# Performance work log

Measured on AMD Instinct MI355X. Metric: run time of the kernel, lower is better.

Reference implementation:

```python
import jax, jax.numpy as jnp
import numpy as np

H = 8          # num_heads
EPS = 1e-5     # nn.LayerNorm default eps


def _attn(x, kv, wq, bq, wk, bk, wv, bv, wo, bo):
    # x: [B, Nq, D] queries; kv: [B, Nk, D] keys/values. softmax over keys (dim=-1).
    B, Nq, D = x.shape
    Nk = kv.shape[1]
    d = D // H
    q = (x @ wq + bq).reshape(B, Nq, H, d).transpose(0, 2, 1, 3)   # [B,h,Nq,d]
    k = (kv @ wk + bk).reshape(B, Nk, H, d).transpose(0, 2, 1, 3)  # [B,h,Nk,d]
    v = (kv @ wv + bv).reshape(B, Nk, H, d).transpose(0, 2, 1, 3)  # [B,h,Nk,d]
    scores = jnp.einsum('bhqd,bhkd->bhqk', q, k) * (d ** -0.5)
    a = jax.nn.softmax(scores, axis=-1)                            # softmax_dim='keys'
    ctx = jnp.einsum('bhqk,bhkd->bhqd', a, v)
    ctx = ctx.transpose(0, 2, 1, 3).reshape(B, Nq, D)
    return ctx @ wo + bo


def _ln(x, g, b):
    mu = jnp.mean(x, axis=-1, keepdims=True)
    var = jnp.var(x, axis=-1, keepdims=True)  # biased, matches torch LayerNorm
    return (x - mu) * jax.lax.rsqrt(var + EPS) * g + b


def setup_inputs() -> dict:
    key = jax.random.key(0)
    B, Nq, Nk, D = 2, 2048, 4096, 512
    Hid = 4 * D
    ks = jax.random.split(key, 32)
    s = 0.02
    r = lambda i, shp: jax.random.normal(ks[i], shp, dtype=jnp.float32) * s
    inp = {
        'x': jax.random.normal(ks[0], (B, Nq, D), dtype=jnp.float32),
        'cross': jax.random.normal(ks[1], (B, Nk, D), dtype=jnp.float32),
        # cross-attention projections (stored as [in, out])
        'ca_wq': r(2, (D, D)), 'ca_bq': jnp.zeros((D,), jnp.float32),
        'ca_wk': r(3, (D, D)), 'ca_bk': jnp.zeros((D,), jnp.float32),
        'ca_wv': r(4, (D, D)), 'ca_bv': jnp.zeros((D,), jnp.float32),
        'ca_wo': r(5, (D, D)), 'ca_bo': jnp.zeros((D,), jnp.float32),
        # self-attention projections
        'sa_wq': r(6, (D, D)), 'sa_bq': jnp.zeros((D,), jnp.float32),
        'sa_wk': r(7, (D, D)), 'sa_bk': jnp.zeros((D,), jnp.float32),
        'sa_wv': r(8, (D, D)), 'sa_bv': jnp.zeros((D,), jnp.float32),
        'sa_wo': r(9, (D, D)), 'sa_bo': jnp.zeros((D,), jnp.float32),
        # layer norms
        'ln1_g': jnp.ones((D,), jnp.float32), 'ln1_b': jnp.zeros((D,), jnp.float32),
        'ln2_g': jnp.ones((D,), jnp.float32), 'ln2_b': jnp.zeros((D,), jnp.float32),
        # MLP
        'mlp_w1': r(10, (D, Hid)), 'mlp_b1': jnp.zeros((Hid,), jnp.float32),
        'mlp_w2': r(11, (Hid, D)), 'mlp_b2': jnp.zeros((D,), jnp.float32),
    }
    return inp


def reference(x, cross,
              ca_wq, ca_bq, ca_wk, ca_bk, ca_wv, ca_bv, ca_wo, ca_bo,
              sa_wq, sa_bq, sa_wk, sa_bk, sa_wv, sa_bv, sa_wo, sa_bo,
              ln1_g, ln1_b, ln2_g, ln2_b,
              mlp_w1, mlp_b1, mlp_w2, mlp_b2):
    # a) cross-attention
    xc = _attn(x, cross, ca_wq, ca_bq, ca_wk, ca_bk, ca_wv, ca_bv, ca_wo, ca_bo)
    # b,c) LN then self-attention (Q=K=V=ln1(xc))
    xn = _ln(xc, ln1_g, ln1_b)
    xs = _attn(xn, xn, sa_wq, sa_bq, sa_wk, sa_bk, sa_wv, sa_bv, sa_wo, sa_bo)
    # d) residual
    y = xc + xs
    # e,f) LN + GELU MLP (torch GELU default = exact erf)
    h1 = jax.nn.gelu(_ln(y, ln2_g, ln2_b) @ mlp_w1 + mlp_b1, approximate=False)
    z = h1 @ mlp_w2 + mlp_b2
    # g) residual
    return y + z
```

## Files before the change

### kernel.cpp

```cpp
#include <hip/hip_runtime.h>
#include <math.h>

typedef _Float16 f16;
typedef __attribute__((ext_vector_type(8))) _Float16 f16x8;
typedef __attribute__((ext_vector_type(4))) _Float16 f16x4;
typedef __attribute__((ext_vector_type(4))) float f32x4;

#define QSCALE 0.1803368801111204f

__device__ __forceinline__ void gl_lds16(const f16* g, f16* l) {
    __builtin_amdgcn_global_load_lds((const __attribute__((address_space(1))) void*)g,
                                     (__attribute__((address_space(3))) void*)l, 16, 0, 0);
}

__global__ __launch_bounds__(256)
void cvt_f16_kernel(const float* __restrict__ X, f16* __restrict__ Y) {
    size_t i = ((size_t)blockIdx.x * 256 + threadIdx.x) * 4;
    f32x4 v = *(const f32x4*)(X + i);
    f16x4 o;
    o[0] = (f16)v[0]; o[1] = (f16)v[1]; o[2] = (f16)v[2]; o[3] = (f16)v[3];
    *(f16x4*)(Y + i) = o;
}

__global__ __launch_bounds__(256)
void transpose_cvt(const float* __restrict__ W, f16* __restrict__ Wt, int K, int N) {
    __shared__ float t[32][33];
    int tx = threadIdx.x, ty = threadIdx.y;
    int n0 = blockIdx.x * 32, k0 = blockIdx.y * 32;
#pragma unroll
    for (int i = 0; i < 4; i++)
        t[ty + i * 8][tx] = W[(size_t)(k0 + ty + i * 8) * N + n0 + tx];
    __syncthreads();
#pragma unroll
    for (int i = 0; i < 4; i++)
        Wt[(size_t)(n0 + ty + i * 8) * K + k0 + tx] = (f16)t[tx][ty + i * 8];
}

struct P8 { const float* s[8]; f16* d[8]; };
__global__ __launch_bounds__(256)
void transpose_cvt8(P8 p) {
    __shared__ float t[32][33];
    const float* W = p.s[blockIdx.z];
    f16* Wt = p.d[blockIdx.z];
    int tx = threadIdx.x, ty = threadIdx.y;
    int n0 = blockIdx.x * 32, k0 = blockIdx.y * 32;
#pragma unroll
    for (int i = 0; i < 4; i++)
        t[ty + i * 8][tx] = W[(size_t)(k0 + ty + i * 8) * 512 + n0 + tx];
    __syncthreads();
#pragma unroll
    for (int i = 0; i < 4; i++)
        Wt[(size_t)(n0 + ty + i * 8) * 512 + k0 + tx] = (f16)t[tx][ty + i * 8];
}

__global__ __launch_bounds__(256)
void transpose_v(const f16* __restrict__ Vh, f16* __restrict__ Vt, int Nk) {
    __shared__ f16 t[64][72];
    int bh = blockIdx.y, k0 = blockIdx.x * 64;
    int tid = threadIdx.x;
    int kr = tid >> 2, dc = (tid & 3) * 16;
    const f16* src = Vh + ((size_t)bh * Nk + k0 + kr) * 64 + dc;
    f16x8 a = *(const f16x8*)src;
    f16x8 b = *(const f16x8*)(src + 8);
    *(f16x8*)&t[kr][dc] = a;
    *(f16x8*)&t[kr][dc + 8] = b;
    __syncthreads();
    int dr = tid >> 2, kc = (tid & 3) * 16;
    f16x8 o0, o1;
#pragma unroll
    for (int j = 0; j < 8; j++) { o0[j] = t[kc + j][dr]; o1[j] = t[kc + 8 + j][dr]; }
    f16* dst = Vt + ((size_t)bh * 64 + dr) * Nk + k0 + kc;
    *(f16x8*)dst = o0;
    *(f16x8*)(dst + 8) = o1;
}

__global__ __launch_bounds__(128)
void layernorm_f16(const float* __restrict__ X, const float* __restrict__ g,
                   const float* __restrict__ bta, f16* __restrict__ Y)
{
    __shared__ float red[4];
    int row = blockIdx.x;
    int tid = threadIdx.x;
    const float* x = X + (size_t)row * 512;
    f32x4 v = *(const f32x4*)(x + tid * 4);
    float s  = v[0] + v[1] + v[2] + v[3];
    float ss = v[0] * v[0] + v[1] * v[1] + v[2] * v[2] + v[3] * v[3];
#pragma unroll
    for (int m = 1; m < 64; m <<= 1) {
        s  += __shfl_xor(s, m, 64);
        ss += __shfl_xor(ss, m, 64);
    }
    int wave = tid >> 6, lane = tid & 63;
    if (lane == 0) { red[wave * 2] = s; red[wave * 2 + 1] = ss; }
    __syncthreads();
    s = red[0] + red[2]; ss = red[1] + red[3];
    float mu  = s * (1.0f / 512);
    float var = ss * (1.0f / 512) - mu * mu;
    float inv = rsqrtf(var + 1e-5f);
    f32x4 gv = *(const f32x4*)(g + tid * 4);
    f32x4 bv = *(const f32x4*)(bta + tid * 4);
    f16x4 o;
#pragma unroll
    for (int i = 0; i < 4; i++) o[i] = (f16)((v[i] - mu) * inv * gv[i] + bv[i]);
    *(f16x4*)(Y + (size_t)row * 512 + tid * 4) = o;
}

__global__ __launch_bounds__(256)
void gemm_f16(const f16* __restrict__ A, const f16* __restrict__ Wt,
              const float* __restrict__ b0, const float* __restrict__ b1,
              const float* __restrict__ b2, const float* __restrict__ res,
              float* __restrict__ Cf32, f16* __restrict__ C16,
              f16* __restrict__ hm0, f16* __restrict__ hm1, f16* __restrict__ hm2,
              int N, int K, int NBshift, int fused, int act, float s0)
{
    __shared__ __align__(16) f16 As[128 * 64];
    __shared__ __align__(16) f16 Bs[128 * 64];
    int tid = threadIdx.x, lane = tid & 63, wave = tid >> 6;
    int quad = lane >> 4, ln16 = lane & 15;
    int wm = wave >> 1, wn = wave & 1;
    int bm0 = blockIdx.y * 128, bn0 = blockIdx.x * 128;

    f32x4 acc[4][4];
#pragma unroll
    for (int i = 0; i < 4; i++)
#pragma unroll
        for (int j = 0; j < 4; j++) acc[i][j] = (f32x4){0.f, 0.f, 0.f, 0.f};

    const f16* ag[4]; const f16* bg[4]; f16* al[4]; f16* bl[4];
#pragma unroll
    for (int j = 0; j < 4; j++) {
        int L = tid + j * 256;
        int row = L >> 3, cc = (L & 7) ^ (row & 7);
        ag[j] = A  + (size_t)(bm0 + row) * K + cc * 8;
        bg[j] = Wt + (size_t)(bn0 + row) * K + cc * 8;
        al[j] = As + (size_t)L * 8;
        bl[j] = Bs + (size_t)L * 8;
    }
    int sw0 = (quad ^ (ln16 & 7)) * 8, sw1 = ((4 + quad) ^ (ln16 & 7)) * 8;

    for (int kt = 0; kt < K; kt += 64) {
        __syncthreads();
#pragma unroll
        for (int j = 0; j < 4; j++) gl_lds16(ag[j], al[j]);
#pragma unroll
        for (int j = 0; j < 4; j++) gl_lds16(bg[j], bl[j]);
        __syncthreads();
#pragma unroll
        for (int h = 0; h < 2; h++) {
            int sw = h ? sw1 : sw0;
            f16x8 af[4], bf[4];
#pragma unroll
            for (int mt = 0; mt < 4; mt++)
                af[mt] = *(const f16x8*)&As[(wm * 64 + mt * 16 + ln16) * 64 + sw];
#pragma unroll
            for (int nt = 0; nt < 4; nt++)
                bf[nt] = *(const f16x8*)&Bs[(wn * 64 + nt * 16 + ln16) * 64 + sw];
#pragma unroll
            for (int mt = 0; mt < 4; mt++)
#pragma unroll
                for (int nt = 0; nt < 4; nt++)
                    acc[mt][nt] = __builtin_amdgcn_mfma_f32_16x16x32_f16(af[mt], bf[nt], acc[mt][nt], 0, 0, 0);
        }
#pragma unroll
        for (int j = 0; j < 4; j++) { ag[j] += 64; bg[j] += 64; }
    }

    int NB = 1 << NBshift;
#pragma unroll
    for (int mt = 0; mt < 4; mt++) {
#pragma unroll
        for (int nt = 0; nt < 4; nt++) {
            int row = bm0 + wm * 64 + mt * 16 + quad * 4;
            int col = bn0 + wn * 64 + nt * 16 + ln16;
            float bv;
            if (fused) {
                int seg = col >> 9;
                const float* bp = seg == 0 ? b0 : (seg == 1 ? b1 : b2);
                bv = bp[col & 511];
            } else bv = b0[col];
#pragma unroll
            for (int i = 0; i < 4; i++) {
                int r = row + i;
                float v = acc[mt][nt][i] + bv;
                size_t idx = (size_t)r * N + col;
                if (res) v += res[idx];
                if (act) v = 0.5f * v * (1.0f + erff(v * 0.70710678118654752f));
                if (Cf32) Cf32[idx] = v;
                if (C16) C16[idx] = (f16)v;
                if (hm0) {
                    int seg = col >> 9;
                    f16* hp = seg == 0 ? hm0 : (seg == 1 ? hm1 : hm2);
                    float vv = seg == 0 ? v * s0 : v;
                    int hh = (col >> 6) & 7, d = col & 63;
                    int bt = r >> NBshift, rr = r & (NB - 1);
                    hp[(((size_t)bt * 8 + hh) * NB + rr) * 64 + d] = (f16)vv;
                }
            }
        }
    }
}

__global__ __launch_bounds__(256)
void gemm64(const f16* __restrict__ A, const f16* __restrict__ Wt,
            const float* __restrict__ bias, const float* __restrict__ res,
            float* __restrict__ Cf32, f16* __restrict__ hm0,
            int N, int K, int NBshift, float s0)
{
    __shared__ __align__(16) f16 As[64 * 64];
    __shared__ __align__(16) f16 Bs[64 * 64];
    int tid = threadIdx.x, lane = tid & 63, wave = tid >> 6;
    int quad = lane >> 4, ln16 = lane & 15;
    int wm = wave >> 1, wn = wave & 1;
    int bm0 = blockIdx.y * 64, bn0 = blockIdx.x * 64;

    f32x4 acc[2][2];
#pragma unroll
    for (int i = 0; i < 2; i++)
#pragma unroll
        for (int j = 0; j < 2; j++) acc[i][j] = (f32x4){0.f, 0.f, 0.f, 0.f};

    const f16* ag[2]; const f16* bg[2]; f16* al[2]; f16* bl[2];
#pragma unroll
    for (int j = 0; j < 2; j++) {
        int L = tid + j * 256;
        int row = L >> 3, cc = (L & 7) ^ (row & 7);
        ag[j] = A  + (size_t)(bm0 + row) * K + cc * 8;
        bg[j] = Wt + (size_t)(bn0 + row) * K + cc * 8;
        al[j] = As + (size_t)L * 8;
        bl[j] = Bs + (size_t)L * 8;
    }
    int sw0 = (quad ^ (ln16 & 7)) * 8, sw1 = ((4 + quad) ^ (ln16 & 7)) * 8;

    for (int kt = 0; kt < K; kt += 64) {
        __syncthreads();
#pragma unroll
        for (int j = 0; j < 2; j++) gl_lds16(ag[j], al[j]);
#pragma unroll
        for (int j = 0; j < 2; j++) gl_lds16(bg[j], bl[j]);
        __syncthreads();
#pragma unroll
        for (int h = 0; h < 2; h++) {
            int sw = h ? sw1 : sw0;
            f16x8 af[2], bf[2];
#pragma unroll
            for (int mt = 0; mt < 2; mt++)
                af[mt] = *(const f16x8*)&As[(wm * 32 + mt * 16 + ln16) * 64 + sw];
#pragma unroll
            for (int nt = 0; nt < 2; nt++)
                bf[nt] = *(const f16x8*)&Bs[(wn * 32 + nt * 16 + ln16) * 64 + sw];
#pragma unroll
            for (int mt = 0; mt < 2; mt++)
#pragma unroll
                for (int nt = 0; nt < 2; nt++)
                    acc[mt][nt] = __builtin_amdgcn_mfma_f32_16x16x32_f16(af[mt], bf[nt], acc[mt][nt], 0, 0, 0);
        }
#pragma unroll
        for (int j = 0; j < 2; j++) { ag[j] += 64; bg[j] += 64; }
    }

    int NB = 1 << NBshift;
#pragma unroll
    for (int mt = 0; mt < 2; mt++) {
#pragma unroll
        for (int nt = 0; nt < 2; nt++) {
            int row = bm0 + wm * 32 + mt * 16 + quad * 4;
            int col = bn0 + wn * 32 + nt * 16 + ln16;
            float bv = bias[col];
#pragma unroll
            for (int i = 0; i < 4; i++) {
                int r = row + i;
                float v = acc[mt][nt][i] + bv;
                size_t idx = (size_t)r * N + col;
                if (res) v += res[idx];
                if (Cf32) Cf32[idx] = v;
                if (hm0) {
                    int hh = (col >> 6) & 7, d = col & 63;
                    int bt = r >> NBshift, rr = r & (NB - 1);
                    hm0[(((size_t)bt * 8 + hh) * NB + rr) * 64 + d] = (f16)(v * s0);
                }
            }
        }
    }
}

__global__ __launch_bounds__(256, 4)
void attention_split(const f16* __restrict__ Qh, const f16* __restrict__ Kh,
                     const f16* __restrict__ Vt, f16* __restrict__ Op,
                     float2* __restrict__ ML, int Nk)
{
    __shared__ __align__(16) f16 Kt[64 * 64];
    __shared__ __align__(16) f16 Vs[64 * 64];
    __shared__ __align__(16) f16 Ps[4][16 * 136];
    int z = blockIdx.z;
    int b = z >> 1, sp = z & 1;
    int h = blockIdx.y, bh = b * 8 + h;
    int Nkh = Nk >> 1;
    int tid = threadIdx.x, lane = tid & 63, wave = tid >> 6;
    int quad = lane >> 4, ln16 = lane & 15;
    int qrow0 = blockIdx.x * 64 + wave * 16;

    f16x8 aq0, aq1;
    {
        const f16* qp = Qh + ((size_t)bh * 2048 + qrow0 + ln16) * 64 + quad * 8;
        aq0 = *(const f16x8*)qp;
        aq1 = *(const f16x8*)(qp + 32);
    }
    f16x8 ones;
#pragma unroll
    for (int j = 0; j < 8; j++) ones[j] = (f16)1.0f;

    float mrun[4];
    f32x4 oacc[4], aol = (f32x4){0.f, 0.f, 0.f, 0.f};
#pragma unroll
    for (int i = 0; i < 4; i++) { mrun[i] = -INFINITY; oacc[i] = (f32x4){0.f, 0.f, 0.f, 0.f}; }

    const f16* kb = Kh + ((size_t)bh * Nk + sp * Nkh) * 64;
    const f16* vb = Vt + (size_t)bh * 64 * Nk + sp * Nkh;

    int L0 = tid, L1 = tid + 256;
    const f16* kg0 = kb + (size_t)(L0 >> 3) * 64 + ((L0 & 7) ^ ((L0 >> 3) & 7)) * 8;
    const f16* kg1 = kb + (size_t)(L1 >> 3) * 64 + ((L1 & 7) ^ ((L1 >> 3) & 7)) * 8;
    const f16* vg0 = vb + (size_t)(L0 >> 3) * Nk + ((L0 & 7) ^ ((L0 >> 3) & 7)) * 8;
    const f16* vg1 = vb + (size_t)(L1 >> 3) * Nk + ((L1 & 7) ^ ((L1 >> 3) & 7)) * 8;
    f16* kl0 = Kt + (size_t)L0 * 8; f16* kl1 = Kt + (size_t)L1 * 8;
    f16* vl0 = Vs + (size_t)L0 * 8; f16* vl1 = Vs + (size_t)L1 * 8;

    int ko0[4], ko1[4], vo[4][2];
#pragma unroll
    for (int nt = 0; nt < 4; nt++) {
        int key = nt * 16 + ln16;
        ko0[nt] = key * 64 + (quad ^ (key & 7)) * 8;
        ko1[nt] = key * 64 + ((4 + quad) ^ (key & 7)) * 8;
    }
#pragma unroll
    for (int dt = 0; dt < 4; dt++) {
        int d = dt * 16 + ln16;
#pragma unroll
        for (int kk = 0; kk < 2; kk++)
            vo[dt][kk] = d * 64 + (((kk * 4 + quad) ^ (d & 7)) * 8);
    }
    int pr0 = ln16 * 136 + quad * 8, pr1 = pr0 + 32;

    for (int kt = 0; kt < Nkh; kt += 64) {
        __syncthreads();
        gl_lds16(kg0, kl0); gl_lds16(kg1, kl1);
        gl_lds16(vg0, vl0); gl_lds16(vg1, vl1);
        __syncthreads();
        kg0 += 64 * 64; kg1 += 64 * 64;
        vg0 += 64; vg1 += 64;

        f32x4 s[4];
#pragma unroll
        for (int nt = 0; nt < 4; nt++) {
            f16x8 kb0 = *(const f16x8*)&Kt[ko0[nt]];
            f16x8 kb1 = *(const f16x8*)&Kt[ko1[nt]];
            f32x4 zz = (f32x4){0.f, 0.f, 0.f, 0.f};
            zz = __builtin_amdgcn_mfma_f32_16x16x32_f16(aq0, kb0, zz, 0, 0, 0);
            zz = __builtin_amdgcn_mfma_f32_16x16x32_f16(aq1, kb1, zz, 0, 0, 0);
            s[nt] = zz;
        }
        float mx[4];
#pragma unroll
        for (int i = 0; i < 4; i++)
            mx[i] = fmaxf(fmaxf(s[0][i], s[1][i]), fmaxf(s[2][i], s[3][i]));
#pragma unroll
        for (int m = 1; m < 16; m <<= 1)
#pragma unroll
            for (int i = 0; i < 4; i++) mx[i] = fmaxf(mx[i], __shfl_xor(mx[i], m, 64));
        float alpha[4];
#pragma unroll
        for (int i = 0; i < 4; i++) {
            float mn = fmaxf(mrun[i], mx[i]);
            alpha[i] = exp2f(mrun[i] - mn);
            mrun[i] = mn;
        }
        f16* pw = &Ps[wave][0];
#pragma unroll
        for (int nt = 0; nt < 4; nt++)
#pragma unroll
            for (int i = 0; i < 4; i++)
                pw[(quad * 4 + i) * 136 + nt * 16 + ln16] = (f16)exp2f(s[nt][i] - mrun[i]);
#pragma unroll
        for (int dt = 0; dt < 4; dt++)
#pragma unroll
            for (int i = 0; i < 4; i++) oacc[dt][i] *= alpha[i];
#pragma unroll
        for (int i = 0; i < 4; i++) aol[i] *= alpha[i];

        f16x8 ap0 = *(const f16x8*)&pw[pr0];
        f16x8 ap1 = *(const f16x8*)&pw[pr1];
        aol = __builtin_amdgcn_mfma_f32_16x16x32_f16(ap0, ones, aol, 0, 0, 0);
        aol = __builtin_amdgcn_mfma_f32_16x16x32_f16(ap1, ones, aol, 0, 0, 0);
#pragma unroll
        for (int dt = 0; dt < 4; dt++) {
            f16x8 vb0 = *(const f16x8*)&Vs[vo[dt][0]];
            f16x8 vb1 = *(const f16x8*)&Vs[vo[dt][1]];
            oacc[dt] = __builtin_amdgcn_mfma_f32_16x16x32_f16(ap0, vb0, oacc[dt], 0, 0, 0);
            oacc[dt] = __builtin_amdgcn_mfma_f32_16x16x32_f16(ap1, vb1, oacc[dt], 0, 0, 0);
        }
    }

    int qb = qrow0 + quad * 4;
    size_t pb = (size_t)(sp * 16 + bh) * 2048;
#pragma unroll
    for (int dt = 0; dt < 4; dt++)
#pragma unroll
        for (int i = 0; i < 4; i++)
            Op[(pb + qb + i) * 64 + dt * 16 + ln16] = (f16)oacc[dt][i];
    if (ln16 == 0) {
#pragma unroll
        for (int i = 0; i < 4; i++) {
            float2 ml; ml.x = mrun[i]; ml.y = aol[i];
            ML[pb + qb + i] = ml;
        }
    }
}

__global__ __launch_bounds__(256)
void attn_combine(const f16* __restrict__ Op, const float2* __restrict__ ML,
                  f16* __restrict__ O)
{
    int t = blockIdx.x * 256 + threadIdx.x;
    int d = t & 63;
    int q = (t >> 6) & 2047;
    int bh = t >> 17;
    int b = bh >> 3, h = bh & 7;
    size_t i0 = (size_t)bh * 2048 + q;
    size_t i1 = (size_t)(16 + bh) * 2048 + q;
    float2 ml0 = ML[i0], ml1 = ML[i1];
    float m = fmaxf(ml0.x, ml1.x);
    float e0 = exp2f(ml0.x - m), e1 = exp2f(ml1.x - m);
    float l = e0 * ml0.y + e1 * ml1.y;
    float o0 = (float)Op[i0 * 64 + d], o1 = (float)Op[i1 * 64 + d];
    float val = (e0 * o0 + e1 * o1) / l;
    O[((size_t)b * 2048 + q) * 512 + h * 64 + d] = (f16)val;
}

extern "C" void kernel_launch(void* const* d_in, const int* in_sizes, int n_in,
                              void* d_out, int out_size, void* d_ws, size_t ws_size,
                              hipStream_t stream)
{
    (void)in_sizes; (void)n_in; (void)out_size; (void)ws_size;
    const float* x      = (const float*)d_in[0];
    const float* cross  = (const float*)d_in[1];
    const float* ca_wq  = (const float*)d_in[2];
    const float* ca_bq  = (const float*)d_in[3];
    const float* ca_wk  = (const float*)d_in[4];
    const float* ca_bk  = (const float*)d_in[5];
    const float* ca_wv  = (const float*)d_in[6];
    const float* ca_bv  = (const float*)d_in[7];
    const float* ca_wo  = (const float*)d_in[8];
    const float* ca_bo  = (const float*)d_in[9];
    const float* sa_wq  = (const float*)d_in[10];
    const float* sa_bq  = (const float*)d_in[11];
    const float* sa_wk  = (const float*)d_in[12];
    const float* sa_bk  = (const float*)d_in[13];
    const float* sa_wv  = (const float*)d_in[14];
    const float* sa_bv  = (const float*)d_in[15];
    const float* sa_wo  = (const float*)d_in[16];
    const float* sa_bo  = (const float*)d_in[17];
    const float* ln1_g  = (const float*)d_in[18];
    const float* ln1_b  = (const float*)d_in[19];
    const float* ln2_g  = (const float*)d_in[20];
    const float* ln2_b  = (const float*)d_in[21];
    const float* mlp_w1 = (const float*)d_in[22];
    const float* mlp_b1 = (const float*)d_in[23];
    const float* mlp_w2 = (const float*)d_in[24];
    const float* mlp_b2 = (const float*)d_in[25];
    float* out = (float*)d_out;

    float* XC = (float*)d_ws;
    float* Yb = XC + 2097152;
    f16* fb   = (f16*)(Yb + 2097152);
    f16* xh     = fb;
    f16* crossh = xh + 2097152;
    f16* xnh    = crossh + 4194304;
    f16* xn2h   = xnh + 2097152;
    f16* Qh     = xn2h + 2097152;
    f16* Kh     = Qh + 2097152;
    f16* Vh     = Kh + 4194304;
    f16* Vtb    = Vh + 4194304;
    f16* ctxh   = Vtb + 4194304;
    f16* h1h    = ctxh + 2097152;
    f16* t_caq  = h1h + 8388608;
    f16* t_cak  = t_caq + 262144;
    f16* t_cav  = t_cak + 262144;
    f16* t_cao  = t_cav + 262144;
    f16* t_saq  = t_cao + 262144;
    f16* t_sak  = t_saq + 262144;
    f16* t_sav  = t_sak + 262144;
    f16* t_sao  = t_sav + 262144;
    f16* t_w1   = t_sao + 262144;
    f16* t_w2   = t_w1 + 1048576;
    float2* ML  = (float2*)(t_w2 + 1048576);

    dim3 tb(32, 8);
    P8 p8;
    p8.s[0] = ca_wq; p8.d[0] = t_caq;
    p8.s[1] = ca_wk; p8.d[1] = t_cak;
    p8.s[2] = ca_wv; p8.d[2] = t_cav;
    p8.s[3] = ca_wo; p8.d[3] = t_cao;
    p8.s[4] = sa_wq; p8.d[4] = t_saq;
    p8.s[5] = sa_wk; p8.d[5] = t_sak;
    p8.s[6] = sa_wv; p8.d[6] = t_sav;
    p8.s[7] = sa_wo; p8.d[7] = t_sao;
    transpose_cvt8<<<dim3(16, 16, 8), tb, 0, stream>>>(p8);
    transpose_cvt<<<dim3(64, 16), tb, 0, stream>>>(mlp_w1, t_w1, 512, 2048);
    transpose_cvt<<<dim3(16, 64), tb, 0, stream>>>(mlp_w2, t_w2, 2048, 512);
    cvt_f16_kernel<<<2048, 256, 0, stream>>>(x, xh);
    cvt_f16_kernel<<<4096, 256, 0, stream>>>(cross, crossh);

    gemm64<<<dim3(8, 64), 256, 0, stream>>>(xh, t_caq, ca_bq, nullptr, nullptr, Qh,
                                            512, 512, 11, QSCALE);
    gemm_f16<<<dim3(8, 64), 256, 0, stream>>>(crossh, t_cak, ca_bk, ca_bv, nullptr, nullptr,
        nullptr, nullptr, Kh, Vh, nullptr, 1024, 512, 12, 1, 0, 1.0f);
    transpose_v<<<dim3(64, 16), 256, 0, stream>>>(Vh, Vtb, 4096);
    attention_split<<<dim3(32, 8, 4), 256, 0, stream>>>(Qh, Kh, Vtb, Vh, ML, 4096);
    attn_combine<<<8192, 256, 0, stream>>>(Vh, ML, ctxh);
    gemm64<<<dim3(8, 64), 256, 0, stream>>>(ctxh, t_cao, ca_bo, nullptr, XC, nullptr,
                                            512, 512, 11, 1.0f);
    layernorm_f16<<<4096, 128, 0, stream>>>(XC, ln1_g, ln1_b, xnh);
    gemm_f16<<<dim3(12, 32), 256, 0, stream>>>(xnh, t_saq, sa_bq, sa_bk, sa_bv, nullptr,
        nullptr, nullptr, Qh, Kh, Vh, 1536, 512, 11, 1, 0, QSCALE);
    transpose_v<<<dim3(32, 16), 256, 0, stream>>>(Vh, Vtb, 2048);
    attention_split<<<dim3(32, 8, 4), 256, 0, stream>>>(Qh, Kh, Vtb, Vh, ML, 2048);
    attn_combine<<<8192, 256, 0, stream>>>(Vh, ML, ctxh);
    gemm64<<<dim3(8, 64), 256, 0, stream>>>(ctxh, t_sao, sa_bo, XC, Yb, nullptr,
                                            512, 512, 11, 1.0f);
    layernorm_f16<<<4096, 128, 0, stream>>>(Yb, ln2_g, ln2_b, xn2h);
    gemm_f16<<<dim3(16, 32), 256, 0, stream>>>(xn2h, t_w1, mlp_b1, nullptr, nullptr, nullptr,
        nullptr, h1h, nullptr, nullptr, nullptr, 2048, 512, 11, 0, 1, 1.0f);
    gemm64<<<dim3(8, 64), 256, 0, stream>>>(h1h, t_w2, mlp_b2, Yb, out, nullptr,
                                            512, 2048, 11, 1.0f);
}
```

Before: 433.1 us.

## Restructure split attention: two waves of 32 query rows, transposed S=K·Q MFMA

The attention kernel now runs 128 threads (2 waves), each wave handling 32 query rows, so K and V fragments loaded from LDS are reused across two 16-row query tiles. Scores are computed transposed (K as A operand, Q as B), so each lane owns one query row. That lets the row max and sum reduce with two cross-quad shuffles instead of four-step shuffles. Row sums are now accumulated in registers rather than through an extra MFMA against a ones vector, and P is stored to a swizzled LDS buffer with packed 4-wide writes. The trade-off is more register pressure and fewer threads per block for the cooperative K/V loads, with the occupancy hint removed from the launch bounds.

```diff
diff --git a/kernel.cpp b/kernel.cpp
--- a/kernel.cpp
+++ b/kernel.cpp
@@ -283,135 +283,154 @@
     }
 }
 
-__global__ __launch_bounds__(256, 4)
+__global__ __launch_bounds__(128)
 void attention_split(const f16* __restrict__ Qh, const f16* __restrict__ Kh,
                      const f16* __restrict__ Vt, f16* __restrict__ Op,
                      float2* __restrict__ ML, int Nk)
 {
     __shared__ __align__(16) f16 Kt[64 * 64];
     __shared__ __align__(16) f16 Vs[64 * 64];
-    __shared__ __align__(16) f16 Ps[4][16 * 136];
-    int z = blockIdx.z;
-    int b = z >> 1, sp = z & 1;
+    __shared__ __align__(16) f16 Ps[2 * 32 * 64];
+    int z = blockIdx.z, b = z >> 1, sp = z & 1;
     int h = blockIdx.y, bh = b * 8 + h;
     int Nkh = Nk >> 1;
     int tid = threadIdx.x, lane = tid & 63, wave = tid >> 6;
-    int quad = lane >> 4, ln16 = lane & 15;
-    int qrow0 = blockIdx.x * 64 + wave * 16;
-
-    f16x8 aq0, aq1;
-    {
-        const f16* qp = Qh + ((size_t)bh * 2048 + qrow0 + ln16) * 64 + quad * 8;
-        aq0 = *(const f16x8*)qp;
-        aq1 = *(const f16x8*)(qp + 32);
-    }
-    f16x8 ones;
-#pragma unroll
-    for (int j = 0; j < 8; j++) ones[j] = (f16)1.0f;
-
-    float mrun[4];
-    f32x4 oacc[4], aol = (f32x4){0.f, 0.f, 0.f, 0.f};
-#pragma unroll
-    for (int i = 0; i < 4; i++) { mrun[i] = -INFINITY; oacc[i] = (f32x4){0.f, 0.f, 0.f, 0.f}; }
+    int quad = lane >> 4, ln16 = lane & 15, l7 = ln16 & 7;
+    int qrow0 = blockIdx.x * 64 + wave * 32;
+
+    f16x8 qf[2][2];
+#pragma unroll
+    for (int qh = 0; qh < 2; qh++)
+#pragma unroll
+        for (int dh = 0; dh < 2; dh++)
+            qf[qh][dh] = *(const f16x8*)(Qh + ((size_t)bh * 2048 + qrow0 + qh * 16 + ln16) * 64
+                                         + dh * 32 + quad * 8);
+
+    float mrun[2] = {-INFINITY, -INFINITY};
+    float lrun[2] = {0.f, 0.f};
+    f32x4 oacc[2][4];
+#pragma unroll
+    for (int qh = 0; qh < 2; qh++)
+#pragma unroll
+        for (int dt = 0; dt < 4; dt++) oacc[qh][dt] = (f32x4){0.f, 0.f, 0.f, 0.f};
 
     const f16* kb = Kh + ((size_t)bh * Nk + sp * Nkh) * 64;
     const f16* vb = Vt + (size_t)bh * 64 * Nk + sp * Nkh;
 
-    int L0 = tid, L1 = tid + 256;
-    const f16* kg0 = kb + (size_t)(L0 >> 3) * 64 + ((L0 & 7) ^ ((L0 >> 3) & 7)) * 8;
-    const f16* kg1 = kb + (size_t)(L1 >> 3) * 64 + ((L1 & 7) ^ ((L1 >> 3) & 7)) * 8;
-    const f16* vg0 = vb + (size_t)(L0 >> 3) * Nk + ((L0 & 7) ^ ((L0 >> 3) & 7)) * 8;
-    const f16* vg1 = vb + (size_t)(L1 >> 3) * Nk + ((L1 & 7) ^ ((L1 >> 3) & 7)) * 8;
-    f16* kl0 = Kt + (size_t)L0 * 8; f16* kl1 = Kt + (size_t)L1 * 8;
-    f16* vl0 = Vs + (size_t)L0 * 8; f16* vl1 = Vs + (size_t)L1 * 8;
-
-    int ko0[4], ko1[4], vo[4][2];
-#pragma unroll
-    for (int nt = 0; nt < 4; nt++) {
-        int key = nt * 16 + ln16;
-        ko0[nt] = key * 64 + (quad ^ (key & 7)) * 8;
-        ko1[nt] = key * 64 + ((4 + quad) ^ (key & 7)) * 8;
-    }
-#pragma unroll
-    for (int dt = 0; dt < 4; dt++) {
-        int d = dt * 16 + ln16;
-#pragma unroll
-        for (int kk = 0; kk < 2; kk++)
-            vo[dt][kk] = d * 64 + (((kk * 4 + quad) ^ (d & 7)) * 8);
-    }
-    int pr0 = ln16 * 136 + quad * 8, pr1 = pr0 + 32;
+    const f16* kg[4]; const f16* vg[4]; f16* kl[4]; f16* vl[4];
+#pragma unroll
+    for (int j = 0; j < 4; j++) {
+        int L = tid + j * 128;
+        int row = L >> 3, cc = (L & 7) ^ (row & 7);
+        kg[j] = kb + (size_t)row * 64 + cc * 8;
+        vg[j] = vb + (size_t)row * Nk + cc * 8;
+        kl[j] = Kt + (size_t)L * 8;
+        vl[j] = Vs + (size_t)L * 8;
+    }
+
+    int koff[4][2], voff[4][2], poff_r[2][2];
+#pragma unroll
+    for (int nt = 0; nt < 4; nt++)
+#pragma unroll
+        for (int dh = 0; dh < 2; dh++)
+            koff[nt][dh] = (nt * 16 + ln16) * 64 + ((dh * 4 + quad) ^ l7) * 8;
+#pragma unroll
+    for (int dt = 0; dt < 4; dt++)
+#pragma unroll
+        for (int c = 0; c < 2; c++)
+            voff[dt][c] = (dt * 16 + ln16) * 64 + ((c * 4 + quad) ^ l7) * 8;
+    int pbase = wave * 2048;
+#pragma unroll
+    for (int qh = 0; qh < 2; qh++)
+#pragma unroll
+        for (int c = 0; c < 2; c++)
+            poff_r[qh][c] = pbase + (qh * 16 + ln16) * 64 + ((c * 4 + quad) ^ l7) * 8;
+    int pw_half = (quad & 1) * 4;
+    int pw_rowc = quad >> 1;
 
     for (int kt = 0; kt < Nkh; kt += 64) {
         __syncthreads();
-        gl_lds16(kg0, kl0); gl_lds16(kg1, kl1);
-        gl_lds16(vg0, vl0); gl_lds16(vg1, vl1);
+#pragma unroll
+        for (int j = 0; j < 4; j++) gl_lds16(kg[j], kl[j]);
+#pragma unroll
+        for (int j = 0; j < 4; j++) gl_lds16(vg[j], vl[j]);
         __syncthreads();
-        kg0 += 64 * 64; kg1 += 64 * 64;
-        vg0 += 64; vg1 += 64;
-
-        f32x4 s[4];
-#pragma unroll
-        for (int nt = 0; nt < 4; nt++) {
-            f16x8 kb0 = *(const f16x8*)&Kt[ko0[nt]];
-            f16x8 kb1 = *(const f16x8*)&Kt[ko1[nt]];
-            f32x4 zz = (f32x4){0.f, 0.f, 0.f, 0.f};
-            zz = __builtin_amdgcn_mfma_f32_16x16x32_f16(aq0, kb0, zz, 0, 0, 0);
-            zz = __builtin_amdgcn_mfma_f32_16x16x32_f16(aq1, kb1, zz, 0, 0, 0);
-            s[nt] = zz;
-        }
-        float mx[4];
-#pragma unroll
-        for (int i = 0; i < 4; i++)
-            mx[i] = fmaxf(fmaxf(s[0][i], s[1][i]), fmaxf(s[2][i], s[3][i]));
-#pragma unroll
-        for (int m = 1; m < 16; m <<= 1)
-#pragma unroll
-            for (int i = 0; i < 4; i++) mx[i] = fmaxf(mx[i], __shfl_xor(mx[i], m, 64));
-        float alpha[4];
-#pragma unroll
-        for (int i = 0; i < 4; i++) {
-            float mn = fmaxf(mrun[i], mx[i]);
-            alpha[i] = exp2f(mrun[i] - mn);
-            mrun[i] = mn;
-        }
-        f16* pw = &Ps[wave][0];
+#pragma unroll
+        for (int j = 0; j < 4; j++) { kg[j] += 64 * 64; vg[j] += 64; }
+
+        f16x8 kf[4][2], vf[4][2];
 #pragma unroll
         for (int nt = 0; nt < 4; nt++)
 #pragma unroll
-            for (int i = 0; i < 4; i++)
-                pw[(quad * 4 + i) * 136 + nt * 16 + ln16] = (f16)exp2f(s[nt][i] - mrun[i]);
+            for (int dh = 0; dh < 2; dh++)
+                kf[nt][dh] = *(const f16x8*)&Kt[koff[nt][dh]];
 #pragma unroll
         for (int dt = 0; dt < 4; dt++)
 #pragma unroll
-            for (int i = 0; i < 4; i++) oacc[dt][i] *= alpha[i];
-#pragma unroll
-        for (int i = 0; i < 4; i++) aol[i] *= alpha[i];
-
-        f16x8 ap0 = *(const f16x8*)&pw[pr0];
-        f16x8 ap1 = *(const f16x8*)&pw[pr1];
-        aol = __builtin_amdgcn_mfma_f32_16x16x32_f16(ap0, ones, aol, 0, 0, 0);
-        aol = __builtin_amdgcn_mfma_f32_16x16x32_f16(ap1, ones, aol, 0, 0, 0);
+            for (int c = 0; c < 2; c++)
+                vf[dt][c] = *(const f16x8*)&Vs[voff[dt][c]];
+
+#pragma unroll
+        for (int qh = 0; qh < 2; qh++) {
+            f32x4 st[4];
+#pragma unroll
+            for (int nt = 0; nt < 4; nt++) {
+                f32x4 zz = (f32x4){0.f, 0.f, 0.f, 0.f};
+                zz = __builtin_amdgcn_mfma_f32_16x16x32_f16(kf[nt][0], qf[qh][0], zz, 0, 0, 0);
+                zz = __builtin_amdgcn_mfma_f32_16x16x32_f16(kf[nt][1], qf[qh][1], zz, 0, 0, 0);
+                st[nt] = zz;
+            }
+            float mx = fmaxf(fmaxf(fmaxf(st[0][0], st[0][1]), fmaxf(st[0][2], st[0][3])),
+                             fmaxf(fmaxf(st[1][0], st[1][1]), fmaxf(st[1][2], st[1][3])));
+            float m2 = fmaxf(fmaxf(fmaxf(st[2][0], st[2][1]), fmaxf(st[2][2], st[2][3])),
+                             fmaxf(fmaxf(st[3][0], st[3][1]), fmaxf(st[3][2], st[3][3])));
+            mx = fmaxf(mx, m2);
+            mx = fmaxf(mx, __shfl_xor(mx, 16, 64));
+            mx = fmaxf(mx, __shfl_xor(mx, 32, 64));
+            float mn = fmaxf(mrun[qh], mx);
+            float alpha = exp2f(mrun[qh] - mn);
+            mrun[qh] = mn;
+            float rs = 0.f;
+            int prow = pbase + (qh * 16 + ln16) * 64;
+#pragma unroll
+            for (int nt = 0; nt < 4; nt++) {
+                float e0 = exp2f(st[nt][0] - mn), e1 = exp2f(st[nt][1] - mn);
+                float e2 = exp2f(st[nt][2] - mn), e3 = exp2f(st[nt][3] - mn);
+                rs += (e0 + e1) + (e2 + e3);
+                f16x4 pk;
+                pk[0] = (f16)e0; pk[1] = (f16)e1; pk[2] = (f16)e2; pk[3] = (f16)e3;
+                *(f16x4*)&Ps[prow + ((nt * 2 + pw_rowc) ^ l7) * 8 + pw_half] = pk;
+            }
+            rs += __shfl_xor(rs, 16, 64);
+            rs += __shfl_xor(rs, 32, 64);
+            lrun[qh] = lrun[qh] * alpha + rs;
+#pragma unroll
+            for (int dt = 0; dt < 4; dt++)
+#pragma unroll
+                for (int i = 0; i < 4; i++) oacc[qh][dt][i] *= alpha;
+            f16x8 pf0 = *(const f16x8*)&Ps[poff_r[qh][0]];
+            f16x8 pf1 = *(const f16x8*)&Ps[poff_r[qh][1]];
+#pragma unroll
+            for (int dt = 0; dt < 4; dt++) {
+                oacc[qh][dt] = __builtin_amdgcn_mfma_f32_16x16x32_f16(vf[dt][0], pf0, oacc[qh][dt], 0, 0, 0);
+                oacc[qh][dt] = __builtin_amdgcn_mfma_f32_16x16x32_f16(vf[dt][1], pf1, oacc[qh][dt], 0, 0, 0);
+            }
+        }
+    }
+
+#pragma unroll
+    for (int qh = 0; qh < 2; qh++) {
+        size_t rowb = ((size_t)(sp * 16 + bh) * 2048 + qrow0 + qh * 16 + ln16) * 64;
 #pragma unroll
         for (int dt = 0; dt < 4; dt++) {
-            f16x8 vb0 = *(const f16x8*)&Vs[vo[dt][0]];
-            f16x8 vb1 = *(const f16x8*)&Vs[vo[dt][1]];
-            oacc[dt] = __builtin_amdgcn_mfma_f32_16x16x32_f16(ap0, vb0, oacc[dt], 0, 0, 0);
-            oacc[dt] = __builtin_amdgcn_mfma_f32_16x16x32_f16(ap1, vb1, oacc[dt], 0, 0, 0);
-        }
-    }
-
-    int qb = qrow0 + quad * 4;
-    size_t pb = (size_t)(sp * 16 + bh) * 2048;
-#pragma unroll
-    for (int dt = 0; dt < 4; dt++)
-#pragma unroll
-        for (int i = 0; i < 4; i++)
-            Op[(pb + qb + i) * 64 + dt * 16 + ln16] = (f16)oacc[dt][i];
-    if (ln16 == 0) {
-#pragma unroll
-        for (int i = 0; i < 4; i++) {
-            float2 ml; ml.x = mrun[i]; ml.y = aol[i];
-            ML[pb + qb + i] = ml;
+            f16x4 o4;
+#pragma unroll
+            for (int i = 0; i < 4; i++) o4[i] = (f16)oacc[qh][dt][i];
+            *(f16x4*)&Op[rowb + dt * 16 + quad * 4] = o4;
+        }
+        if (quad == 0) {
+            float2 ml; ml.x = mrun[qh]; ml.y = lrun[qh];
+            ML[(size_t)(sp * 16 + bh) * 2048 + qrow0 + qh * 16 + ln16] = ml;
         }
     }
 }
@@ -515,7 +534,7 @@
     gemm_f16<<<dim3(8, 64), 256, 0, stream>>>(crossh, t_cak, ca_bk, ca_bv, nullptr, nullptr,
         nullptr, nullptr, Kh, Vh, nullptr, 1024, 512, 12, 1, 0, 1.0f);
     transpose_v<<<dim3(64, 16), 256, 0, stream>>>(Vh, Vtb, 4096);
-    attention_split<<<dim3(32, 8, 4), 256, 0, stream>>>(Qh, Kh, Vtb, Vh, ML, 4096);
+    attention_split<<<dim3(32, 8, 4), 128, 0, stream>>>(Qh, Kh, Vtb, Vh, ML, 4096);
     attn_combine<<<8192, 256, 0, stream>>>(Vh, ML, ctxh);
     gemm64<<<dim3(8, 64), 256, 0, stream>>>(ctxh, t_cao, ca_bo, nullptr, XC, nullptr,
                                             512, 512, 11, 1.0f);
@@ -523,7 +542,7 @@
     gemm_f16<<<dim3(12, 32), 256, 0, stream>>>(xnh, t_saq, sa_bq, sa_bk, sa_bv, nullptr,
         nullptr, nullptr, Qh, Kh, Vh, 1536, 512, 11, 1, 0, QSCALE);
     transpose_v<<<dim3(32, 16), 256, 0, stream>>>(Vh, Vtb, 2048);
-    attention_split<<<dim3(32, 8, 4), 256, 0, stream>>>(Qh, Kh, Vtb, Vh, ML, 2048);
+    attention_split<<<dim3(32, 8, 4), 128, 0, stream>>>(Qh, Kh, Vtb, Vh, ML, 2048);
     attn_combine<<<8192, 256, 0, stream>>>(Vh, ML, ctxh);
     gemm64<<<dim3(8, 64), 256, 0, stream>>>(ctxh, t_sao, sa_bo, XC, Yb, nullptr,
                                             512, 512, 11, 1.0f);
```

New measurement: 465.2 us. 1.07x slower.
